# Optimization experiments

Measured on AMD Instinct MI355X. Metric: run time of the kernel, lower is better.

The kernel has to match this reference:

```python
import jax, jax.numpy as jnp
import numpy as np

N = 100000   # nodes
E = 1600000  # edges
D = 128      # out_feats
V = 5000     # annotation_size
L = 3        # n_steps SAGE layers


def setup_inputs() -> dict:
    key = jax.random.key(0)
    k0, k1, k2, k3, k4 = jax.random.split(key, 5)
    annotation = jax.random.randint(k0, (N,), 0, V)
    src = jax.random.randint(k1, (E,), 0, N)
    dst = jax.random.randint(k2, (E,), 0, N)
    emb = jax.random.normal(k3, (V, D), dtype=jnp.float32) * 0.02
    Ws = jax.random.normal(k4, (L, D, D), dtype=jnp.float32) / np.sqrt(D).astype(np.float32)
    bs = jnp.zeros((L, D), dtype=jnp.float32)
    return {"annotation": annotation, "src": src, "dst": dst, "emb": emb, "Ws": Ws, "bs": bs}


def reference(annotation, src, dst, emb, Ws, bs):
    # tok_embedding == 2: embedding lookup of node token ids
    h = emb[annotation]                                              # [N, D]
    # in-degree per destination node (constant across layers)
    deg = jax.ops.segment_sum(jnp.ones_like(src, dtype=jnp.float32), dst, num_segments=N)
    inv = 1.0 / (deg + 1.0)                                          # [N]
    # DGL SAGEConv, aggregator_type='gcn', eval mode (feat_drop is identity):
    #   h_neigh = (h_self + sum_{u->v} h_u) / (in_deg + 1); rst = relu(h_neigh @ W + b)
    for l in range(L):
        agg = jax.ops.segment_sum(h[src], dst, num_segments=N)       # [N, D] gather-scatter
        h = jax.nn.relu(((h + agg) * inv[:, None]) @ Ws[l] + bs[l])
    # residual=False -> merged node features are just h ('_merge_on nodes h')
    return h
```

## Files before the change

### kernel.cpp

```cpp
#include <hip/hip_runtime.h>
#include <hip/hip_fp16.h>


#define D 128
#define PBLK 128
#define BSH 7

typedef float f32x4 __attribute__((ext_vector_type(4)));
typedef _Float16 f16x8 __attribute__((ext_vector_type(8)));

__global__ __launch_bounds__(256) void k_hist(
    const int* __restrict__ dst, int* __restrict__ hist,
    int E, int chunk, int nbk) {
    __shared__ int lh[1024];
    int j = blockIdx.x, tid = threadIdx.x;
    for (int i = tid; i < nbk; i += 256) lh[i] = 0;
    __syncthreads();
    int e0 = j * chunk, e1 = min(E, e0 + chunk);
    for (int e = e0 + tid; e < e1; e += 256)
        atomicAdd(&lh[dst[e] >> BSH], 1);
    __syncthreads();
    for (int i = tid; i < nbk; i += 256) hist[(size_t)j * nbk + i] = lh[i];
}

__global__ void k_scan_offs(int* __restrict__ hist, int* __restrict__ tot, int nbk) {
    __shared__ int s[PBLK];
    int b = blockIdx.x, j = threadIdx.x;
    int v = hist[(size_t)j * nbk + b];
    s[j] = v;
    __syncthreads();
    for (int off = 1; off < PBLK; off <<= 1) {
        int x = (j >= off) ? s[j - off] : 0;
        __syncthreads();
        s[j] += x;
        __syncthreads();
    }
    hist[(size_t)j * nbk + b] = s[j] - v;
    if (j == PBLK - 1) tot[b] = s[j];
}

__global__ void k_scan_tot(int* __restrict__ tot, int* __restrict__ row_ptr,
                           int nbk, int N, int E) {
    __shared__ int s[1024];
    int t = threadIdx.x;
    int v = (t < nbk) ? tot[t] : 0;
    s[t] = v;
    __syncthreads();
    for (int off = 1; off < 1024; off <<= 1) {
        int x = (t >= off) ? s[t - off] : 0;
        __syncthreads();
        s[t] += x;
        __syncthreads();
    }
    if (t < nbk) tot[t] = s[t] - v;
    if (t == 0) { tot[nbk] = E; row_ptr[N] = E; }
}

__global__ __launch_bounds__(256) void k_scatter(
    const int* __restrict__ src, const int* __restrict__ dst,
    const int* __restrict__ ann, const int* __restrict__ hist,
    const int* __restrict__ tot, int2* __restrict__ tmp,
    int E, int chunk, int nbk) {
    __shared__ int cur[1024];
    int j = blockIdx.x, tid = threadIdx.x;
    for (int i = tid; i < nbk; i += 256)
        cur[i] = tot[i] + hist[(size_t)j * nbk + i];
    __syncthreads();
    int e0 = j * chunk, e1 = min(E, e0 + chunk);
    for (int e = e0 + tid; e < e1; e += 256) {
        int d = dst[e], s = src[e];
        int p = atomicAdd(&cur[d >> BSH], 1);
        tmp[p] = make_int2(s, ((d & ((1 << BSH) - 1)) << 13) | ann[s]);
    }
}

__global__ __launch_bounds__(256) void k_place(
    const int2* __restrict__ tmp, const int* __restrict__ tot,
    int* __restrict__ row_ptr, int2* __restrict__ eal, int N) {
    __shared__ int cnt[1 << BSH], sc[1 << BSH];
    int b = blockIdx.x, tid = threadIdx.x;
    int base = tot[b], end = tot[b + 1];
    if (tid < (1 << BSH)) cnt[tid] = 0;
    __syncthreads();
    for (int i = base + tid; i < end; i += 256)
        atomicAdd(&cnt[((unsigned)tmp[i].y) >> 13], 1);
    __syncthreads();
    if (tid < (1 << BSH)) sc[tid] = cnt[tid];
    __syncthreads();
    for (int off = 1; off < (1 << BSH); off <<= 1) {
        int x = (tid < (1 << BSH) && tid >= off) ? sc[tid - off] : 0;
        __syncthreads();
        if (tid < (1 << BSH)) sc[tid] += x;
        __syncthreads();
    }
    if (tid < (1 << BSH)) {
        int excl = sc[tid] - cnt[tid];
        int d0 = (b << BSH) + tid;
        if (d0 < N) row_ptr[d0] = base + excl;
        cnt[tid] = excl;
    }
    __syncthreads();
    for (int i = base + tid; i < end; i += 256) {
        int2 w = tmp[i];
        int p = atomicAdd(&cnt[((unsigned)w.y) >> 13], 1);
        eal[base + p] = make_int2(w.x, w.y & 0x1FFF);
    }
}

union H16Chunk { float4 f4; __half2 h2[4]; __half h[8]; };

__global__ void k_h16(const float* __restrict__ x, __half* __restrict__ y, int n8) {
    int i = blockIdx.x * blockDim.x + threadIdx.x;
    if (i >= n8) return;
    const float4* p = (const float4*)x;
    float4 a = p[2 * i], b = p[2 * i + 1];
    H16Chunk u;
    u.h2[0] = __floats2half2_rn(a.x, a.y);
    u.h2[1] = __floats2half2_rn(a.z, a.w);
    u.h2[2] = __floats2half2_rn(b.x, b.y);
    u.h2[3] = __floats2half2_rn(b.z, b.w);
    *(float4*)&y[8 * i] = u.f4;
}

#define XT_LD 136
__global__ __launch_bounds__(256) void k_gemm_mfma(
    const __half* __restrict__ x16, const float* __restrict__ W,
    __half* __restrict__ g16, int n, int ntiles) {
    __shared__ __half Bf[8 * 4 * 64 * 8];
    __shared__ __half Xt[64 * XT_LD];
    int tid = threadIdx.x;
    int lane = tid & 63;
    int wv = tid >> 6;

    for (int idx = tid; idx < 8 * 4 * 64; idx += 256) {
        int l = idx & 63, ks = (idx >> 6) & 3, nt = idx >> 8;
        int kq = (l >> 4) * 8;
        int col = nt * 16 + (l & 15);
        H16Chunk u;
        #pragma unroll
        for (int j = 0; j < 8; j++)
            u.h[j] = __float2half(W[(ks * 32 + kq + j) * 128 + col]);
        *(float4*)&Bf[idx * 8] = u.f4;
    }
    __syncthreads();

    f16x8 breg[8][4];
    #pragma unroll
    for (int nt = 0; nt < 8; nt++)
        #pragma unroll
        for (int ks = 0; ks < 4; ks++)
            breg[nt][ks] = *(f16x8*)&Bf[((nt * 4 + ks) * 64 + lane) * 8];

    int srow = tid >> 2;
    int sc = (tid & 3) * 32;
    int m = lane & 15, quad = lane >> 4;

    for (int tile = blockIdx.x; tile < ntiles; tile += gridDim.x) {
        int row0 = tile * 64;
        __syncthreads();
        {
            int gr = row0 + srow;
            if (gr >= n) gr = n - 1;
            const float4* xp = (const float4*)&x16[(size_t)gr * 128 + sc];
            float4 v0 = xp[0], v1 = xp[1], v2 = xp[2], v3 = xp[3];
            float4* xd = (float4*)&Xt[srow * XT_LD + sc];
            xd[0] = v0; xd[1] = v1; xd[2] = v2; xd[3] = v3;
        }
        __syncthreads();

        f32x4 acc[8];
        #pragma unroll
        for (int nt = 0; nt < 8; nt++) acc[nt] = (f32x4){0.f, 0.f, 0.f, 0.f};
        #pragma unroll
        for (int ks = 0; ks < 4; ks++) {
            f16x8 a = *(f16x8*)&Xt[(wv * 16 + m) * XT_LD + ks * 32 + quad * 8];
            #pragma unroll
            for (int nt = 0; nt < 8; nt++)
                acc[nt] = __builtin_amdgcn_mfma_f32_16x16x32_f16(a, breg[nt][ks], acc[nt], 0, 0, 0);
        }
        __syncthreads();
        #pragma unroll
        for (int nt = 0; nt < 8; nt++)
            #pragma unroll
            for (int r = 0; r < 4; r++)
                Xt[(wv * 16 + quad * 4 + r) * XT_LD + nt * 16 + m] = __float2half(acc[nt][r]);
        __syncthreads();
        {
            int gr = row0 + srow;
            if (gr < n) {
                float4* gp = (float4*)&g16[(size_t)gr * 128 + sc];
                float4* xs = (float4*)&Xt[srow * XT_LD + sc];
                gp[0] = xs[0]; gp[1] = xs[1]; gp[2] = xs[2]; gp[3] = xs[3];
            }
        }
    }
}

template<bool SELY>
__global__ __launch_bounds__(512) void k_agg_gemm(
    const float4* __restrict__ tab, const int* __restrict__ selfidx,
    const int* __restrict__ row_ptr, const int2* __restrict__ eal,
    const float4* __restrict__ bias4, const float* __restrict__ W,
    __half* __restrict__ g16, int n, int ntiles) {
    __shared__ __half Bf[8 * 4 * 64 * 8];
    __shared__ __half Xt[64 * XT_LD];
    int tid = threadIdx.x;
    int lane = tid & 63;
    int wv = tid >> 6;
    int unit = tid >> 4;
    int ul = tid & 15;

    for (int idx = tid; idx < 8 * 4 * 64; idx += 512) {
        int l = idx & 63, ks = (idx >> 6) & 3, nt = idx >> 8;
        int kq = (l >> 4) * 8;
        int col = nt * 16 + (l & 15);
        H16Chunk u;
        #pragma unroll
        for (int j = 0; j < 8; j++)
            u.h[j] = __float2half(W[(ks * 32 + kq + j) * 128 + col]);
        *(float4*)&Bf[idx * 8] = u.f4;
    }
    __syncthreads();

    int m = lane & 15, quad = lane >> 4;
    int stripe = wv >> 1;
    int ntb = (wv & 1) * 4;

    #define ACCUMK(A, raw) do { H16Chunk u; u.f4 = (raw);                      \
        float2 t0 = __half22float2(u.h2[0]); A[0] += t0.x; A[1] += t0.y;       \
        float2 t1 = __half22float2(u.h2[1]); A[2] += t1.x; A[3] += t1.y;       \
        float2 t2 = __half22float2(u.h2[2]); A[4] += t2.x; A[5] += t2.y;       \
        float2 t3 = __half22float2(u.h2[3]); A[6] += t3.x; A[7] += t3.y; } while (0)
    #define IDX(w) (SELY ? (w).y : (w).x)

    for (int tile = blockIdx.x; tile < ntiles; tile += gridDim.x) {
        int row0 = tile * 64;
        float acc[2][8] = {};
        int degk[2];
        #pragma unroll
        for (int k = 0; k < 2; k++) {
            int r = unit * 2 + k;
            int v = row0 + r;
            int vv = (v < n) ? v : 0;
            int beg = row_ptr[vv];
            int end = (v < n) ? row_ptr[vv + 1] : beg;
            degk[k] = end - beg;
            int sr = SELY ? selfidx[vv] : vv;
            ACCUMK(acc[k], tab[(size_t)sr * 16 + ul]);
            int p = beg;
            for (; p + 4 <= end; p += 4) {
                int2 w0 = eal[p], w1 = eal[p + 1], w2 = eal[p + 2], w3 = eal[p + 3];
                float4 r0 = tab[(size_t)IDX(w0) * 16 + ul];
                float4 r1 = tab[(size_t)IDX(w1) * 16 + ul];
                float4 r2 = tab[(size_t)IDX(w2) * 16 + ul];
                float4 r3 = tab[(size_t)IDX(w3) * 16 + ul];
                ACCUMK(acc[k], r0); ACCUMK(acc[k], r1);
                ACCUMK(acc[k], r2); ACCUMK(acc[k], r3);
            }
            for (; p < end; p++) ACCUMK(acc[k], tab[(size_t)IDX(eal[p]) * 16 + ul]);
        }
        __syncthreads();
        {
            float4 b0 = bias4[2 * ul], b1 = bias4[2 * ul + 1];
            #pragma unroll
            for (int k = 0; k < 2; k++) {
                int r = unit * 2 + k;
                float sc = 1.0f / (float)(degk[k] + 1);
                H16Chunk u;
                u.h2[0] = __floats2half2_rn(fmaxf(acc[k][0] * sc + b0.x, 0.f),
                                            fmaxf(acc[k][1] * sc + b0.y, 0.f));
                u.h2[1] = __floats2half2_rn(fmaxf(acc[k][2] * sc + b0.z, 0.f),
                                            fmaxf(acc[k][3] * sc + b0.w, 0.f));
                u.h2[2] = __floats2half2_rn(fmaxf(acc[k][4] * sc + b1.x, 0.f),
                                            fmaxf(acc[k][5] * sc + b1.y, 0.f));
                u.h2[3] = __floats2half2_rn(fmaxf(acc[k][6] * sc + b1.z, 0.f),
                                            fmaxf(acc[k][7] * sc + b1.w, 0.f));
                *(float4*)&Xt[r * XT_LD + ul * 8] = u.f4;
            }
        }
        __syncthreads();
        f32x4 cacc[4];
        #pragma unroll
        for (int t = 0; t < 4; t++) cacc[t] = (f32x4){0.f, 0.f, 0.f, 0.f};
        #pragma unroll
        for (int ks = 0; ks < 4; ks++) {
            f16x8 a = *(f16x8*)&Xt[(stripe * 16 + m) * XT_LD + ks * 32 + quad * 8];
            #pragma unroll
            for (int t = 0; t < 4; t++) {
                f16x8 b = *(f16x8*)&Bf[(((ntb + t) * 4 + ks) * 64 + lane) * 8];
                cacc[t] = __builtin_amdgcn_mfma_f32_16x16x32_f16(a, b, cacc[t], 0, 0, 0);
            }
        }
        __syncthreads();
        #pragma unroll
        for (int t = 0; t < 4; t++)
            #pragma unroll
            for (int r4 = 0; r4 < 4; r4++)
                Xt[(stripe * 16 + quad * 4 + r4) * XT_LD + (ntb + t) * 16 + m] =
                    __float2half(cacc[t][r4]);
        __syncthreads();
        {
            int srow = tid >> 3, c = tid & 7;
            int gr = row0 + srow;
            float4 v0 = *(float4*)&Xt[srow * XT_LD + c * 16];
            float4 v1 = *(float4*)&Xt[srow * XT_LD + c * 16 + 8];
            if (gr < n) {
                float4* gp = (float4*)&g16[(size_t)gr * 128 + c * 16];
                gp[0] = v0;
                gp[1] = v1;
            }
        }
    }
    #undef ACCUMK
    #undef IDX
}

template<bool SELY, bool OUT32>
__global__ __launch_bounds__(256) void k_agg(
    const float4* __restrict__ tab, const int* __restrict__ selfidx,
    const int* __restrict__ row_ptr, const int2* __restrict__ eal,
    const float4* __restrict__ bias4,
    __half* __restrict__ h16out, float* __restrict__ f32out, int n) {
    int v = blockIdx.x * 4 + (threadIdx.x >> 6);
    int lane = threadIdx.x & 63;
    int g = lane >> 4;
    int q = lane & 15;
    int beg = row_ptr[v], end = row_ptr[v + 1];
    int deg = end - beg;
    float acc[8] = {};

    #define ACCUM(raw) do { H16Chunk u; u.f4 = (raw);                          \
        float2 t0 = __half22float2(u.h2[0]); acc[0] += t0.x; acc[1] += t0.y;   \
        float2 t1 = __half22float2(u.h2[1]); acc[2] += t1.x; acc[3] += t1.y;   \
        float2 t2 = __half22float2(u.h2[2]); acc[4] += t2.x; acc[5] += t2.y;   \
        float2 t3 = __half22float2(u.h2[3]); acc[6] += t3.x; acc[7] += t3.y; } while (0)
    #define IDX(w) (SELY ? (w).y : (w).x)

    if (g == 0) {
        int sr = SELY ? selfidx[v] : v;
        ACCUM(tab[(size_t)sr * 16 + q]);
    }

    int quads = deg >> 2;
    int p = 0;
    for (; p + 4 <= quads; p += 4) {
        int eb = beg + 4 * p + g;
        int2 w0 = eal[eb + 0], w1 = eal[eb + 4], w2 = eal[eb + 8], w3 = eal[eb + 12];
        float4 r0 = tab[(size_t)IDX(w0) * 16 + q], r1 = tab[(size_t)IDX(w1) * 16 + q];
        float4 r2 = tab[(size_t)IDX(w2) * 16 + q], r3 = tab[(size_t)IDX(w3) * 16 + q];
        ACCUM(r0); ACCUM(r1); ACCUM(r2); ACCUM(r3);
    }
    for (; p < quads; p++) ACCUM(tab[(size_t)IDX(eal[beg + 4 * p + g]) * 16 + q]);
    int tail = deg & 3;
    if (g < tail) ACCUM(tab[(size_t)IDX(eal[beg + 4 * quads + g]) * 16 + q]);
    #undef ACCUM
    #undef IDX

    #pragma unroll
    for (int j = 0; j < 8; j++) {
        acc[j] += __shfl_down(acc[j], 16, 64);
        acc[j] += __shfl_down(acc[j], 32, 64);
    }
    if (g == 0) {
        float sc = 1.0f / (float)(deg + 1);
        float4 b0 = bias4[2 * q], b1 = bias4[2 * q + 1];
        float o[8];
        o[0] = fmaxf(acc[0] * sc + b0.x, 0.f);
        o[1] = fmaxf(acc[1] * sc + b0.y, 0.f);
        o[2] = fmaxf(acc[2] * sc + b0.z, 0.f);
        o[3] = fmaxf(acc[3] * sc + b0.w, 0.f);
        o[4] = fmaxf(acc[4] * sc + b1.x, 0.f);
        o[5] = fmaxf(acc[5] * sc + b1.y, 0.f);
        o[6] = fmaxf(acc[6] * sc + b1.z, 0.f);
        o[7] = fmaxf(acc[7] * sc + b1.w, 0.f);
        if (!OUT32) {
            H16Chunk u;
            u.h2[0] = __floats2half2_rn(o[0], o[1]);
            u.h2[1] = __floats2half2_rn(o[2], o[3]);
            u.h2[2] = __floats2half2_rn(o[4], o[5]);
            u.h2[3] = __floats2half2_rn(o[6], o[7]);
            *(float4*)&h16out[(size_t)v * 128 + q * 8] = u.f4;
        } else {
            f32x4 a = {o[0], o[1], o[2], o[3]};
            f32x4 b = {o[4], o[5], o[6], o[7]};
            __builtin_nontemporal_store(a, (f32x4*)&f32out[(size_t)v * 128 + q * 8]);
            __builtin_nontemporal_store(b, (f32x4*)&f32out[(size_t)v * 128 + q * 8 + 4]);
        }
    }
}

extern "C" void kernel_launch(void* const* d_in, const int* in_sizes, int n_in,
                              void* d_out, int out_size, void* d_ws, size_t ws_size,
                              hipStream_t stream) {
    const int*   ann = (const int*)d_in[0];
    const int*   src = (const int*)d_in[1];
    const int*   dst = (const int*)d_in[2];
    const float* emb = (const float*)d_in[3];
    const float* Ws  = (const float*)d_in[4];
    const float* bs  = (const float*)d_in[5];
    float* out = (float*)d_out;

    const int N = in_sizes[0];
    const int E = in_sizes[1];
    const int V = in_sizes[3] / D;
    const int NT64 = (N + 63) / 64;
    const int VT64 = (V + 63) / 64;
    const int NBK  = (N + (1 << BSH) - 1) >> BSH;
    const int CHK  = (E + PBLK - 1) / PBLK;

    int*  deg     = (int*)d_ws;
    int*  row_ptr = deg + N;
    int*  bsum    = row_ptr + ((N + 1 + 3) & ~3);
    int2* eal     = (int2*)(bsum + 512);
    __half* hA16  = (__half*)(eal + E);
    __half* gB16  = hA16 + (size_t)N * D;
    __half* embW16= gB16 + (size_t)N * D;
    __half* emb16 = embW16 + (size_t)V * D;
    int2* tmp  = (int2*)hA16;
    int*  hist = (int*)gB16;
    int*  tot  = hist + (size_t)PBLK * NBK;

    k_h16<<<(V * D / 8 + 255) / 256, 256, 0, stream>>>(emb, emb16, V * D / 8);
    k_gemm_mfma<<<VT64, 256, 0, stream>>>(emb16, Ws, embW16, V, VT64);

    k_hist<<<PBLK, 256, 0, stream>>>(dst, hist, E, CHK, NBK);
    k_scan_offs<<<NBK, PBLK, 0, stream>>>(hist, tot, NBK);
    k_scan_tot<<<1, 1024, 0, stream>>>(tot, row_ptr, NBK, N, E);
    k_scatter<<<PBLK, 256, 0, stream>>>(src, dst, ann, hist, tot, tmp, E, CHK, NBK);
    k_place<<<NBK, 256, 0, stream>>>(tmp, tot, row_ptr, eal, N);

    k_agg_gemm<true><<<NT64, 512, 0, stream>>>(
        (const float4*)embW16, ann, row_ptr, eal, (const float4*)bs,
        Ws + (size_t)D * D, gB16, N, NT64);

    k_agg_gemm<false><<<NT64, 512, 0, stream>>>(
        (const float4*)gB16, nullptr, row_ptr, eal, (const float4*)(bs + D),
        Ws + (size_t)2 * D * D, hA16, N, NT64);

    k_agg<false, true><<<N / 4, 256, 0, stream>>>(
        (const float4*)hA16, nullptr, row_ptr, eal, (const float4*)(bs + 2 * D),
        nullptr, out, N);
}
```

Measured before the change: 394.4 us.

## Split each row's edge list across four lane groups in fused agg-GEMM kernel

Changes the gather phase of the fused aggregate+GEMM kernel. Previously 16 lanes handled a row and walked its whole edge list serially, two rows per unit. Now a whole wavefront handles one row at a time, with the four 16-lane groups taking interleaved edges and combining their partial sums by cross-lane shuffles. This shortens the per-row dependent gather chain and adds memory-level parallelism, at the cost of shuffle reductions and idle lanes on low-degree tails.

```diff
diff --git a/kernel.cpp b/kernel.cpp
--- a/kernel.cpp
+++ b/kernel.cpp
@@ -207,8 +207,8 @@
     int tid = threadIdx.x;
     int lane = tid & 63;
     int wv = tid >> 6;
-    int unit = tid >> 4;
-    int ul = tid & 15;
+    int g = lane >> 4;
+    int q = lane & 15;
 
     for (int idx = tid; idx < 8 * 4 * 64; idx += 512) {
         int l = idx & 63, ks = (idx >> 6) & 3, nt = idx >> 8;
@@ -222,60 +222,65 @@
     }
     __syncthreads();
 
-    int m = lane & 15, quad = lane >> 4;
     int stripe = wv >> 1;
     int ntb = (wv & 1) * 4;
-
-    #define ACCUMK(A, raw) do { H16Chunk u; u.f4 = (raw);                      \
-        float2 t0 = __half22float2(u.h2[0]); A[0] += t0.x; A[1] += t0.y;       \
-        float2 t1 = __half22float2(u.h2[1]); A[2] += t1.x; A[3] += t1.y;       \
-        float2 t2 = __half22float2(u.h2[2]); A[4] += t2.x; A[5] += t2.y;       \
-        float2 t3 = __half22float2(u.h2[3]); A[6] += t3.x; A[7] += t3.y; } while (0)
+    float4 b0 = bias4[2 * q], b1 = bias4[2 * q + 1];
+
+    #define ACCUM(raw) do { H16Chunk u; u.f4 = (raw);                          \
+        float2 t0 = __half22float2(u.h2[0]); acc[0] += t0.x; acc[1] += t0.y;   \
+        float2 t1 = __half22float2(u.h2[1]); acc[2] += t1.x; acc[3] += t1.y;   \
+        float2 t2 = __half22float2(u.h2[2]); acc[4] += t2.x; acc[5] += t2.y;   \
+        float2 t3 = __half22float2(u.h2[3]); acc[6] += t3.x; acc[7] += t3.y; } while (0)
     #define IDX(w) (SELY ? (w).y : (w).x)
 
     for (int tile = blockIdx.x; tile < ntiles; tile += gridDim.x) {
         int row0 = tile * 64;
-        float acc[2][8] = {};
-        int degk[2];
-        #pragma unroll
-        for (int k = 0; k < 2; k++) {
-            int r = unit * 2 + k;
+        __syncthreads();
+        for (int j = 0; j < 8; j++) {
+            int r = wv * 8 + j;
             int v = row0 + r;
             int vv = (v < n) ? v : 0;
             int beg = row_ptr[vv];
             int end = (v < n) ? row_ptr[vv + 1] : beg;
-            degk[k] = end - beg;
-            int sr = SELY ? selfidx[vv] : vv;
-            ACCUMK(acc[k], tab[(size_t)sr * 16 + ul]);
-            int p = beg;
-            for (; p + 4 <= end; p += 4) {
-                int2 w0 = eal[p], w1 = eal[p + 1], w2 = eal[p + 2], w3 = eal[p + 3];
-                float4 r0 = tab[(size_t)IDX(w0) * 16 + ul];
-                float4 r1 = tab[(size_t)IDX(w1) * 16 + ul];
-                float4 r2 = tab[(size_t)IDX(w2) * 16 + ul];
-                float4 r3 = tab[(size_t)IDX(w3) * 16 + ul];
-                ACCUMK(acc[k], r0); ACCUMK(acc[k], r1);
-                ACCUMK(acc[k], r2); ACCUMK(acc[k], r3);
-            }
-            for (; p < end; p++) ACCUMK(acc[k], tab[(size_t)IDX(eal[p]) * 16 + ul]);
-        }
-        __syncthreads();
-        {
-            float4 b0 = bias4[2 * ul], b1 = bias4[2 * ul + 1];
+            int deg = end - beg;
+            float acc[8] = {};
+            if (g == 0) {
+                int sr = SELY ? selfidx[vv] : vv;
+                ACCUM(tab[(size_t)sr * 16 + q]);
+            }
+            int quads = deg >> 2;
+            int p = 0;
+            for (; p + 4 <= quads; p += 4) {
+                int eb = beg + 4 * p + g;
+                int2 w0 = eal[eb + 0], w1 = eal[eb + 4];
+                int2 w2 = eal[eb + 8], w3 = eal[eb + 12];
+                float4 r0 = tab[(size_t)IDX(w0) * 16 + q];
+                float4 r1 = tab[(size_t)IDX(w1) * 16 + q];
+                float4 r2 = tab[(size_t)IDX(w2) * 16 + q];
+                float4 r3 = tab[(size_t)IDX(w3) * 16 + q];
+                ACCUM(r0); ACCUM(r1); ACCUM(r2); ACCUM(r3);
+            }
+            for (; p < quads; p++) ACCUM(tab[(size_t)IDX(eal[beg + 4 * p + g]) * 16 + q]);
+            int tail = deg & 3;
+            if (g < tail) ACCUM(tab[(size_t)IDX(eal[beg + 4 * quads + g]) * 16 + q]);
+
             #pragma unroll
-            for (int k = 0; k < 2; k++) {
-                int r = unit * 2 + k;
-                float sc = 1.0f / (float)(degk[k] + 1);
+            for (int jj = 0; jj < 8; jj++) {
+                acc[jj] += __shfl_down(acc[jj], 16, 64);
+                acc[jj] += __shfl_down(acc[jj], 32, 64);
+            }
+            if (g == 0) {
+                float sc = 1.0f / (float)(deg + 1);
                 H16Chunk u;
-                u.h2[0] = __floats2half2_rn(fmaxf(acc[k][0] * sc + b0.x, 0.f),
-                                            fmaxf(acc[k][1] * sc + b0.y, 0.f));
-                u.h2[1] = __floats2half2_rn(fmaxf(acc[k][2] * sc + b0.z, 0.f),
-                                            fmaxf(acc[k][3] * sc + b0.w, 0.f));
-                u.h2[2] = __floats2half2_rn(fmaxf(acc[k][4] * sc + b1.x, 0.f),
-                                            fmaxf(acc[k][5] * sc + b1.y, 0.f));
-                u.h2[3] = __floats2half2_rn(fmaxf(acc[k][6] * sc + b1.z, 0.f),
-                                            fmaxf(acc[k][7] * sc + b1.w, 0.f));
-                *(float4*)&Xt[r * XT_LD + ul * 8] = u.f4;
+                u.h2[0] = __floats2half2_rn(fmaxf(acc[0] * sc + b0.x, 0.f),
+                                            fmaxf(acc[1] * sc + b0.y, 0.f));
+                u.h2[1] = __floats2half2_rn(fmaxf(acc[2] * sc + b0.z, 0.f),
+                                            fmaxf(acc[3] * sc + b0.w, 0.f));
+                u.h2[2] = __floats2half2_rn(fmaxf(acc[4] * sc + b1.x, 0.f),
+                                            fmaxf(acc[5] * sc + b1.y, 0.f));
+                u.h2[3] = __floats2half2_rn(fmaxf(acc[6] * sc + b1.z, 0.f),
+                                            fmaxf(acc[7] * sc + b1.w, 0.f));
+                *(float4*)&Xt[r * XT_LD + q * 8] = u.f4;
             }
         }
         __syncthreads();
@@ -284,7 +289,7 @@
         for (int t = 0; t < 4; t++) cacc[t] = (f32x4){0.f, 0.f, 0.f, 0.f};
         #pragma unroll
         for (int ks = 0; ks < 4; ks++) {
-            f16x8 a = *(f16x8*)&Xt[(stripe * 16 + m) * XT_LD + ks * 32 + quad * 8];
+            f16x8 a = *(f16x8*)&Xt[(stripe * 16 + q) * XT_LD + ks * 32 + g * 8];
             #pragma unroll
             for (int t = 0; t < 4; t++) {
                 f16x8 b = *(f16x8*)&Bf[(((ntb + t) * 4 + ks) * 64 + lane) * 8];
@@ -296,7 +301,7 @@
         for (int t = 0; t < 4; t++)
             #pragma unroll
             for (int r4 = 0; r4 < 4; r4++)
-                Xt[(stripe * 16 + quad * 4 + r4) * XT_LD + (ntb + t) * 16 + m] =
+                Xt[(stripe * 16 + g * 4 + r4) * XT_LD + (ntb + t) * 16 + q] =
                     __float2half(cacc[t][r4]);
         __syncthreads();
         {
@@ -311,7 +316,7 @@
             }
         }
     }
-    #undef ACCUMK
+    #undef ACCUM
     #undef IDX
 }
 
```

Result: slower. 455.9 us (+15.6%).
